# Optimization experiments

Hardware: AMD Instinct MI355X
Metric: run time of the kernel (lower is better)

The kernel has to match this reference:

```python
import jax, jax.numpy as jnp
import numpy as np

N_NODES, N_EDGES, N_RELS, D_IN, D_OUT = 50000, 200000, 64, 32, 32


def setup_inputs() -> dict:
    key = jax.random.key(0)
    k1, k2, k3, k4, k5 = jax.random.split(key, 5)
    feat = jax.random.normal(k1, (N_NODES, D_IN), dtype=jnp.float32)
    # learned per-relation projection weights: [R, D_IN, D_OUT]
    weight = jax.random.normal(k2, (N_RELS, D_IN, D_OUT), dtype=jnp.float32) * 0.05
    src = jax.random.randint(k3, (N_EDGES,), 0, N_NODES)
    dst = jax.random.randint(k4, (N_EDGES,), 0, N_NODES)
    etypes = jax.random.randint(k5, (N_EDGES,), 0, N_RELS)
    return {"feat": feat, "weight": weight, "src": src, "dst": dst, "etypes": etypes}


def reference(feat, weight, src, dst, etypes):
    # gather source features and per-edge relation weights (HighMem variant
    # materializes W[etypes] just like torch index_select), then per-edge bmm
    n_nodes = feat.shape[0]
    msg = jnp.einsum('ei,eio->eo', feat[src], weight[etypes])  # [E, D_OUT]
    out = jax.ops.segment_sum(msg, dst, num_segments=n_nodes)  # [N, D_OUT]
    return out
```

## Files before the change

### kernel.cpp

```cpp
#include <hip/hip_runtime.h>


#define D 32

__global__ __launch_bounds__(256) void rgcn_edge_kernel(
    const float* __restrict__ feat,
    const float* __restrict__ weight,
    const int*   __restrict__ src,
    const int*   __restrict__ dst,
    const int*   __restrict__ etypes,
    float*       __restrict__ out,
    int n_edges)
{
    int gid = blockIdx.x * blockDim.x + threadIdx.x;
    int e = gid >> 5;
    int o = gid & 31;
    if (e >= n_edges) return;

    int s = src[e];
    int d = dst[e];
    int r = etypes[e];

    const float* W = weight + (size_t)r * (D * D);

    float fv = feat[(size_t)s * D + o];

    float acc = 0.f;
    #pragma unroll
    for (int i = 0; i < D; ++i) {
        float fi = __shfl(fv, i, 32);
        acc = fmaf(fi, W[i * D + o], acc);
    }

    atomicAdd(&out[(size_t)d * D + o], acc);
}

extern "C" void kernel_launch(void* const* d_in, const int* in_sizes, int n_in,
                              void* d_out, int out_size, void* d_ws, size_t ws_size,
                              hipStream_t stream) {
    const float* feat   = (const float*)d_in[0];
    const float* weight = (const float*)d_in[1];
    const int*   src    = (const int*)d_in[2];
    const int*   dst    = (const int*)d_in[3];
    const int*   etypes = (const int*)d_in[4];
    float*       out    = (float*)d_out;

    int n_edges = in_sizes[2];

    hipMemsetAsync(d_out, 0, (size_t)out_size * sizeof(float), stream);

    long long total_threads = (long long)n_edges * 32;
    int block = 256;
    int grid = (int)((total_threads + block - 1) / block);
    rgcn_edge_kernel<<<grid, block, 0, stream>>>(feat, weight, src, dst, etypes,
                                                 out, n_edges);
}
```

Before: 106.1 us.

## Sort edges by relation and compute messages with bf16 MFMA tiles

```diff
diff --git a/kernel.cpp b/kernel.cpp
--- a/kernel.cpp
+++ b/kernel.cpp
@@ -2,38 +2,140 @@
 
 
 #define D 32
+#define NRELS 64
+#define BPR 16
+
+typedef __bf16 bf16x8 __attribute__((ext_vector_type(8)));
+typedef float  f32x4  __attribute__((ext_vector_type(4)));
+
+
+__global__ __launch_bounds__(256) void hist_kernel(
+    const int* __restrict__ etypes, int n, int* __restrict__ hist)
+{
+    __shared__ int lh[NRELS];
+    int tid = threadIdx.x;
+    if (tid < NRELS) lh[tid] = 0;
+    __syncthreads();
+    for (int e = blockIdx.x * blockDim.x + tid; e < n; e += gridDim.x * blockDim.x)
+        atomicAdd(&lh[etypes[e]], 1);
+    __syncthreads();
+    if (tid < NRELS) atomicAdd(&hist[tid], lh[tid]);
+}
+
+__global__ void scan_kernel(const int* __restrict__ hist,
+                            int* __restrict__ base, int* __restrict__ cursor)
+{
+    int t = threadIdx.x;
+    int v = hist[t];
+    int x = v;
+    #pragma unroll
+    for (int off = 1; off < 64; off <<= 1) {
+        int y = __shfl_up(x, off, 64);
+        if (t >= off) x += y;
+    }
+    base[t] = x - v;
+    cursor[t] = x - v;
+    if (t == 63) base[64] = x;
+}
+
+__global__ __launch_bounds__(256) void scatter_kernel(
+    const int* __restrict__ src, const int* __restrict__ dst,
+    const int* __restrict__ etypes, int n, int* __restrict__ cursor,
+    int* __restrict__ src_s, int* __restrict__ dst_s)
+{
+    __shared__ int lh[NRELS], lb[NRELS];
+    int tid = threadIdx.x;
+    if (tid < NRELS) lh[tid] = 0;
+    __syncthreads();
+    int e = blockIdx.x * blockDim.x + tid;
+    int r = 0, rank = 0;
+    if (e < n) { r = etypes[e]; rank = atomicAdd(&lh[r], 1); }
+    __syncthreads();
+    if (tid < NRELS) lb[tid] = (lh[tid] > 0) ? atomicAdd(&cursor[tid], lh[tid]) : 0;
+    __syncthreads();
+    if (e < n) {
+        int p = lb[r] + rank;
+        src_s[p] = src[e];
+        dst_s[p] = dst[e];
+    }
+}
+
+
+__global__ __launch_bounds__(256) void rgcn_mfma_kernel(
+    const float* __restrict__ feat, const float* __restrict__ weight,
+    const int* __restrict__ base, const int* __restrict__ src_s,
+    const int* __restrict__ dst_s, float* __restrict__ out)
+{
+    int r    = blockIdx.x / BPR;
+    int sub  = blockIdx.x % BPR;
+    int wave = threadIdx.x >> 6;
+    int lane = threadIdx.x & 63;
+    int n    = lane & 15;
+    int quad = lane >> 4;
+
+    int rbase = base[r];
+    int count = base[r + 1] - rbase;
+    if (count <= 0) return;
+    int ntiles = (count + 15) >> 4;
+
+    const float* W = weight + (size_t)r * (D * D);
+    bf16x8 b0, b1;
+    #pragma unroll
+    for (int j = 0; j < 8; ++j) {
+        int k = quad * 8 + j;
+        b0[j] = (__bf16)W[k * D + n];
+        b1[j] = (__bf16)W[k * D + 16 + n];
+    }
+
+    for (int tile = sub * 4 + wave; tile < ntiles; tile += BPR * 4) {
+        int pe = tile * 16 + n;
+        int pc = pe < count ? pe : count - 1;
+        int s  = src_s[rbase + pc];
+        const float4* fp = (const float4*)(feat + (size_t)s * D + quad * 8);
+        float4 fa = fp[0], fb = fp[1];
+        bf16x8 a;
+        a[0] = (__bf16)fa.x; a[1] = (__bf16)fa.y; a[2] = (__bf16)fa.z; a[3] = (__bf16)fa.w;
+        a[4] = (__bf16)fb.x; a[5] = (__bf16)fb.y; a[6] = (__bf16)fb.z; a[7] = (__bf16)fb.w;
+
+        f32x4 zero = {0.f, 0.f, 0.f, 0.f};
+        f32x4 c0 = __builtin_amdgcn_mfma_f32_16x16x32_bf16(a, b0, zero, 0, 0, 0);
+        f32x4 c1 = __builtin_amdgcn_mfma_f32_16x16x32_bf16(a, b1, zero, 0, 0, 0);
+
+        #pragma unroll
+        for (int v = 0; v < 4; ++v) {
+            int m  = quad * 4 + v;
+            int p2 = tile * 16 + m;
+            if (p2 < count) {
+                int d = dst_s[rbase + p2];
+                atomicAdd(out + (size_t)d * D + n,      c0[v]);
+                atomicAdd(out + (size_t)d * D + 16 + n, c1[v]);
+            }
+        }
+    }
+}
+
 
 __global__ __launch_bounds__(256) void rgcn_edge_kernel(
-    const float* __restrict__ feat,
-    const float* __restrict__ weight,
-    const int*   __restrict__ src,
-    const int*   __restrict__ dst,
-    const int*   __restrict__ etypes,
-    float*       __restrict__ out,
-    int n_edges)
+    const float* __restrict__ feat, const float* __restrict__ weight,
+    const int* __restrict__ src, const int* __restrict__ dst,
+    const int* __restrict__ etypes, float* __restrict__ out, int n_edges)
 {
     int gid = blockIdx.x * blockDim.x + threadIdx.x;
     int e = gid >> 5;
     int o = gid & 31;
     if (e >= n_edges) return;
-
-    int s = src[e];
-    int d = dst[e];
-    int r = etypes[e];
-
+    int s = src[e], d = dst[e], r = etypes[e];
     const float* W = weight + (size_t)r * (D * D);
-
     float fv = feat[(size_t)s * D + o];
-
     float acc = 0.f;
     #pragma unroll
     for (int i = 0; i < D; ++i) {
         float fi = __shfl(fv, i, 32);
         acc = fmaf(fi, W[i * D + o], acc);
     }
-
     atomicAdd(&out[(size_t)d * D + o], acc);
 }
+
 
 extern "C" void kernel_launch(void* const* d_in, const int* in_sizes, int n_in,
                               void* d_out, int out_size, void* d_ws, size_t ws_size,
@@ -45,13 +147,33 @@
     const int*   etypes = (const int*)d_in[4];
     float*       out    = (float*)d_out;
 
-    int n_edges = in_sizes[2];
+    int E = in_sizes[2];
 
     hipMemsetAsync(d_out, 0, (size_t)out_size * sizeof(float), stream);
 
-    long long total_threads = (long long)n_edges * 32;
-    int block = 256;
-    int grid = (int)((total_threads + block - 1) / block);
-    rgcn_edge_kernel<<<grid, block, 0, stream>>>(feat, weight, src, dst, etypes,
-                                                 out, n_edges);
+    size_t need = (size_t)(256 + 2 * (size_t)E) * sizeof(int);
+    if (ws_size < need) {
+        long long total = (long long)E * 32;
+        int grid = (int)((total + 255) / 256);
+        rgcn_edge_kernel<<<grid, 256, 0, stream>>>(feat, weight, src, dst,
+                                                   etypes, out, E);
+        return;
+    }
+
+    int* wsi    = (int*)d_ws;
+    int* hist   = wsi;
+    int* basep  = wsi + 64;
+    int* cursor = wsi + 160;
+    int* src_s  = wsi + 256;
+    int* dst_s  = wsi + 256 + E;
+
+    hipMemsetAsync(d_ws, 0, NRELS * sizeof(int), stream);
+
+    int blocks = (E + 255) / 256;
+    hist_kernel<<<blocks, 256, 0, stream>>>(etypes, E, hist);
+    scan_kernel<<<1, 64, 0, stream>>>(hist, basep, cursor);
+    scatter_kernel<<<blocks, 256, 0, stream>>>(src, dst, etypes, E, cursor,
+                                               src_s, dst_s);
+    rgcn_mfma_kernel<<<NRELS * BPR, 256, 0, stream>>>(feat, weight, basep,
+                                                      src_s, dst_s, out);
 }
```

Result: slower. 125.6 us (+18.3%).

## Stage all relation weights in LDS as bf16 and process edges persistently

Applied to the files above, without the earlier changes.

```diff
diff --git a/kernel.cpp b/kernel.cpp
--- a/kernel.cpp
+++ b/kernel.cpp
@@ -2,37 +2,77 @@
 
 
 #define D 32
+#define NRELS 64
+#define RSTRIDE 34
+#define BLOCK 1024
+#define WPB 16
+#define NBLOCKS 256
 
-__global__ __launch_bounds__(256) void rgcn_edge_kernel(
+__global__ __launch_bounds__(BLOCK) void rgcn_ldsw_kernel(
     const float* __restrict__ feat,
     const float* __restrict__ weight,
     const int*   __restrict__ src,
     const int*   __restrict__ dst,
     const int*   __restrict__ etypes,
     float*       __restrict__ out,
-    int n_edges)
+    int n_edges, int chunk)
 {
-    int gid = blockIdx.x * blockDim.x + threadIdx.x;
-    int e = gid >> 5;
-    int o = gid & 31;
-    if (e >= n_edges) return;
+    __shared__ unsigned short lw[NRELS * D * RSTRIDE];
 
-    int s = src[e];
-    int d = dst[e];
-    int r = etypes[e];
+    for (int idx = threadIdx.x; idx < NRELS * D * D; idx += BLOCK) {
+        int r = idx >> 10, rem = idx & 1023;
+        int i = rem >> 5,  o = rem & 31;
+        unsigned int u = __float_as_uint(weight[idx]);
+        unsigned short b = (unsigned short)((u + 0x7fffu + ((u >> 16) & 1u)) >> 16);
+        lw[(r * D + i) * RSTRIDE + o] = b;
+    }
+    __syncthreads();
 
-    const float* W = weight + (size_t)r * (D * D);
+    int lane = threadIdx.x & 63;
+    int wave = threadIdx.x >> 6;
+    int p = lane & 15;
+    int q = lane >> 4;
+    int c = lane & 31;
 
-    float fv = feat[(size_t)s * D + o];
+    int gwave = blockIdx.x * WPB + wave;
+    int begin = gwave * chunk;
+    int end   = begin + chunk;
+    if (end > n_edges) end = n_edges;
 
-    float acc = 0.f;
-    #pragma unroll
-    for (int i = 0; i < D; ++i) {
-        float fi = __shfl(fv, i, 32);
-        acc = fmaf(fi, W[i * D + o], acc);
+    auto process = [&](int e) {
+        int eu = __builtin_amdgcn_readfirstlane(e);
+        int s = src[eu];
+        int d = dst[eu];
+        int r = etypes[eu];
+
+        float fv = feat[(size_t)s * D + c];
+        const unsigned short* wr = lw + r * (D * RSTRIDE);
+
+        float a0 = 0.f, a1 = 0.f;
+        #pragma unroll
+        for (int j = 0; j < 8; ++j) {
+            int i = q * 8 + j;
+            float fi = __shfl(fv, i, 64);
+            unsigned int wb = *(const unsigned int*)(wr + i * RSTRIDE + 2 * p);
+            float w0 = __uint_as_float(wb << 16);
+            float w1 = __uint_as_float(wb & 0xffff0000u);
+            a0 = fmaf(fi, w0, a0);
+            a1 = fmaf(fi, w1, a1);
+        }
+        a0 += __shfl_xor(a0, 16, 64);
+        a0 += __shfl_xor(a0, 32, 64);
+        a1 += __shfl_xor(a1, 16, 64);
+        a1 += __shfl_xor(a1, 32, 64);
+        if (q == 0)      atomicAdd(out + (size_t)d * D + 2 * p,     a0);
+        else if (q == 1) atomicAdd(out + (size_t)d * D + 2 * p + 1, a1);
+    };
+
+    int e = begin;
+    for (; e + 1 < end; e += 2) {
+        process(e);
+        process(e + 1);
     }
-
-    atomicAdd(&out[(size_t)d * D + o], acc);
+    if (e < end) process(e);
 }
 
 extern "C" void kernel_launch(void* const* d_in, const int* in_sizes, int n_in,
@@ -45,13 +85,13 @@
     const int*   etypes = (const int*)d_in[4];
     float*       out    = (float*)d_out;
 
-    int n_edges = in_sizes[2];
+    int E = in_sizes[2];
 
     hipMemsetAsync(d_out, 0, (size_t)out_size * sizeof(float), stream);
 
-    long long total_threads = (long long)n_edges * 32;
-    int block = 256;
-    int grid = (int)((total_threads + block - 1) / block);
-    rgcn_edge_kernel<<<grid, block, 0, stream>>>(feat, weight, src, dst, etypes,
-                                                 out, n_edges);
+    int total_waves = NBLOCKS * WPB;
+    int chunk = (E + total_waves - 1) / total_waves;
+
+    rgcn_ldsw_kernel<<<NBLOCKS, BLOCK, 0, stream>>>(feat, weight, src, dst,
+                                                    etypes, out, E, chunk);
 }
```

Result: slower. 119.6 us (+12.7%).

## Bucket edges by relation per block and compute messages with bf16 MFMA

Applied to the files above, without the earlier changes.

```diff
diff --git a/kernel.cpp b/kernel.cpp
--- a/kernel.cpp
+++ b/kernel.cpp
@@ -2,36 +2,140 @@
 
 
 #define D 32
+#define NRELS 64
+#define BLOCK 512
+#define WPB (BLOCK / 64)
+#define GRID 512
+#define MAXCHUNK BLOCK
+#define MAXTILES (NRELS + MAXCHUNK / 16)
 
-__global__ __launch_bounds__(256) void rgcn_edge_kernel(
+typedef __bf16 bf16x8 __attribute__((ext_vector_type(8)));
+typedef float  f32x4  __attribute__((ext_vector_type(4)));
+
+__global__ __launch_bounds__(BLOCK, 4) void rgcn_fused_kernel(
     const float* __restrict__ feat,
     const float* __restrict__ weight,
     const int*   __restrict__ src,
     const int*   __restrict__ dst,
     const int*   __restrict__ etypes,
     float*       __restrict__ out,
-    int n_edges)
+    int E, int chunk)
+{
+    __shared__ int cnt[NRELS];
+    __shared__ int off[NRELS];
+    __shared__ unsigned short list[MAXCHUNK];
+    __shared__ unsigned short desc[MAXTILES];
+    __shared__ int ntile_sh;
+
+    int tid = threadIdx.x;
+    int gbase = blockIdx.x * chunk;
+
+    if (tid < NRELS) cnt[tid] = 0;
+    __syncthreads();
+
+    int my_r = -1, my_rank = 0;
+    if (tid < chunk && gbase + tid < E) {
+        my_r = etypes[gbase + tid];
+        my_rank = atomicAdd(&cnt[my_r], 1);
+    }
+    __syncthreads();
+
+    if (tid < 64) {
+        int c = cnt[tid];
+        int x = c;
+        #pragma unroll
+        for (int o = 1; o < 64; o <<= 1) {
+            int y = __shfl_up(x, o, 64);
+            if (tid >= o) x += y;
+        }
+        off[tid] = x - c;
+
+        int nt = (c + 15) >> 4;
+        int tx = nt;
+        #pragma unroll
+        for (int o = 1; o < 64; o <<= 1) {
+            int y = __shfl_up(tx, o, 64);
+            if (tid >= o) tx += y;
+        }
+        int tbase = tx - nt;
+        for (int t = 0; t < nt; ++t)
+            desc[tbase + t] = (unsigned short)((tid << 8) | t);
+        if (tid == 63) ntile_sh = tx;
+    }
+    __syncthreads();
+
+    if (my_r >= 0) list[off[my_r] + my_rank] = (unsigned short)tid;
+    int ntiles = ntile_sh;
+    __syncthreads();
+
+    int wave = tid >> 6;
+    int lane = tid & 63;
+    int n    = lane & 15;
+    int quad = lane >> 4;
+
+    for (int ti = wave; ti < ntiles; ti += WPB) {
+        int dsc = desc[ti];
+        int r = dsc >> 8;
+        int t = dsc & 255;
+        int c = cnt[r];
+        int mbase = t * 16;
+        int mcnt = c - mbase; if (mcnt > 16) mcnt = 16;
+        int lbase = off[r] + mbase;
+
+        const float* W = weight + (size_t)r * (D * D);
+        bf16x8 b0, b1;
+        #pragma unroll
+        for (int j = 0; j < 8; ++j) {
+            int k = quad * 8 + j;
+            b0[j] = (__bf16)W[k * D + n];
+            b1[j] = (__bf16)W[k * D + 16 + n];
+        }
+
+        int mm = (n < mcnt) ? n : 0;
+        int le = list[lbase + mm];
+        int s  = src[gbase + le];
+        const float4* fp = (const float4*)(feat + (size_t)s * D + quad * 8);
+        float4 fa = fp[0], fb = fp[1];
+        bf16x8 a;
+        a[0] = (__bf16)fa.x; a[1] = (__bf16)fa.y; a[2] = (__bf16)fa.z; a[3] = (__bf16)fa.w;
+        a[4] = (__bf16)fb.x; a[5] = (__bf16)fb.y; a[6] = (__bf16)fb.z; a[7] = (__bf16)fb.w;
+
+        f32x4 z = {0.f, 0.f, 0.f, 0.f};
+        f32x4 c0 = __builtin_amdgcn_mfma_f32_16x16x32_bf16(a, b0, z, 0, 0, 0);
+        f32x4 c1 = __builtin_amdgcn_mfma_f32_16x16x32_bf16(a, b1, z, 0, 0, 0);
+
+        #pragma unroll
+        for (int v = 0; v < 4; ++v) {
+            int m2 = quad * 4 + v;
+            if (m2 < mcnt) {
+                int le2 = list[lbase + m2];
+                int d = dst[gbase + le2];
+                atomicAdd(out + (size_t)d * D + n,      c0[v]);
+                atomicAdd(out + (size_t)d * D + 16 + n, c1[v]);
+            }
+        }
+    }
+}
+
+
+__global__ __launch_bounds__(256) void rgcn_edge_kernel(
+    const float* __restrict__ feat, const float* __restrict__ weight,
+    const int* __restrict__ src, const int* __restrict__ dst,
+    const int* __restrict__ etypes, float* __restrict__ out, int n_edges)
 {
     int gid = blockIdx.x * blockDim.x + threadIdx.x;
     int e = gid >> 5;
     int o = gid & 31;
     if (e >= n_edges) return;
-
-    int s = src[e];
-    int d = dst[e];
-    int r = etypes[e];
-
+    int s = src[e], d = dst[e], r = etypes[e];
     const float* W = weight + (size_t)r * (D * D);
-
     float fv = feat[(size_t)s * D + o];
-
     float acc = 0.f;
     #pragma unroll
     for (int i = 0; i < D; ++i) {
         float fi = __shfl(fv, i, 32);
         acc = fmaf(fi, W[i * D + o], acc);
     }
-
     atomicAdd(&out[(size_t)d * D + o], acc);
 }
 
@@ -45,13 +149,18 @@
     const int*   etypes = (const int*)d_in[4];
     float*       out    = (float*)d_out;
 
-    int n_edges = in_sizes[2];
+    int E = in_sizes[2];
 
     hipMemsetAsync(d_out, 0, (size_t)out_size * sizeof(float), stream);
 
-    long long total_threads = (long long)n_edges * 32;
-    int block = 256;
-    int grid = (int)((total_threads + block - 1) / block);
-    rgcn_edge_kernel<<<grid, block, 0, stream>>>(feat, weight, src, dst, etypes,
-                                                 out, n_edges);
+    int chunk = (E + GRID - 1) / GRID;
+    if (chunk <= MAXCHUNK) {
+        rgcn_fused_kernel<<<GRID, BLOCK, 0, stream>>>(feat, weight, src, dst,
+                                                      etypes, out, E, chunk);
+    } else {
+        long long total = (long long)E * 32;
+        int grid = (int)((total + 255) / 256);
+        rgcn_edge_kernel<<<grid, 256, 0, stream>>>(feat, weight, src, dst,
+                                                   etypes, out, E);
+    }
 }
```

Measured after the change: 97.04 us. 1.09x faster.
